# Kernel tuning notes

Measured on AMD Instinct MI355X. Metric: run time of the kernel, lower is better.

## Reference

```python
import jax, jax.numpy as jnp
import numpy as np

N = 50000   # nodes
D = 256     # embed_dim
H = 256     # hidden_dim
E = 250000  # edges per relation type
T = 3       # edge types
NEG_SLOPE = 0.2  # PyG GATConv default


def setup_inputs() -> dict:
    key = jax.random.key(0)
    ks = jax.random.split(key, 12)
    s = lambda k, shape: jax.random.normal(k, shape, jnp.float32) * 0.05
    z = jax.random.normal(ks[0], (N, D), jnp.float32)
    ei = jax.random.randint(ks[1], (T, 2, E), 0, N, dtype=jnp.int32)
    W1 = s(ks[2], (T, D, H)); as1 = s(ks[3], (T, H)); ad1 = s(ks[4], (T, H))
    b1 = jnp.zeros((T, H), jnp.float32)
    W2 = s(ks[5], (T, H, H)); as2 = s(ks[6], (T, H)); ad2 = s(ks[7], (T, H))
    b2 = jnp.zeros((T, H), jnp.float32)
    Wh = s(ks[8], (H, 1)); bh = jnp.zeros((1,), jnp.float32)
    return dict(z=z, ei=ei, W1=W1, as1=as1, ad1=ad1, b1=b1,
                W2=W2, as2=as2, ad2=ad2, b2=b2, Wh=Wh, bh=bh)


def gat_conv(x, ei, W, a_s, a_d, b):
    # PyG GATConv, heads=1, no self loops: h = x W; e_ij = leaky_relu(a_s.h_j + a_d.h_i)
    # alpha = softmax over incoming edges of node i; out_i = sum_j alpha_ij h_j + bias
    src, dst = ei[0], ei[1]
    n = x.shape[0]
    h = x @ W                              # [N, H]
    a_src = h @ a_s                        # [N]
    a_dst = h @ a_d                        # [N]
    e = jax.nn.leaky_relu(a_src[src] + a_dst[dst], NEG_SLOPE)   # [E]
    m = jax.ops.segment_max(e, dst, num_segments=n)             # per-dst max
    ex = jnp.exp(e - m[dst])
    den = jax.ops.segment_sum(ex, dst, num_segments=n)
    alpha = ex / den[dst]                                       # [E]
    out = jax.ops.segment_sum(h[src] * alpha[:, None], dst, num_segments=n)
    return out + b


def layer(x, ei, W, a_s, a_d, b):
    # sum of per-type GATConv outputs, then ReLU (matches module)
    outs = jax.vmap(lambda e_, W_, s_, d_, b_: gat_conv(x, e_, W_, s_, d_, b_))(ei, W, a_s, a_d, b)
    return jax.nn.relu(outs.sum(0))


def reference(z, ei, W1, as1, ad1, b1, W2, as2, ad2, b2, Wh, bh):
    h1 = layer(z, ei, W1, as1, ad1, b1)
    h2 = layer(h1, ei, W2, as2, ad2, b2)
    return jax.nn.sigmoid(h2 @ Wh + bh).squeeze(-1)   # [N]
```

## Files before the change

### kernel.cpp

```cpp
#include <hip/hip_runtime.h>

#define GAT_N 50000
#define GAT_D 256
#define GAT_T 3
#define GAT_E 250000
#define GAT_B (GAT_T*GAT_N)
#define GAT_TOTE (GAT_T*GAT_E)
#define GAT_COLS (GAT_T*GAT_D)
#define GAT_SLOPE 0.2f

typedef unsigned short u16;
typedef unsigned int u32;
typedef __attribute__((ext_vector_type(8))) short s16x8;
typedef __attribute__((ext_vector_type(8))) __bf16 bf16x8;
typedef __attribute__((ext_vector_type(4))) float f32x4;
typedef __attribute__((ext_vector_type(4))) u32 u32x4;

__device__ __forceinline__ u16 f2bf(float f) {
    u32 x = __builtin_bit_cast(u32, f);
    u32 r = (x + 0x7fffu + ((x >> 16) & 1u)) >> 16;
    return (u16)r;
}
__device__ __forceinline__ float lo16(u32 w) {
    return __builtin_bit_cast(float, w << 16);
}
__device__ __forceinline__ float hi16(u32 w) {
    return __builtin_bit_cast(float, w & 0xffff0000u);
}

__global__ void gat_prep(const float* __restrict__ W1, const float* __restrict__ W2,
                         const float* __restrict__ z, const float* __restrict__ b1,
                         const float* __restrict__ b2, u16* __restrict__ WT1b,
                         u16* __restrict__ WT2b, u16* __restrict__ zb,
                         u32* __restrict__ cnt, u32* __restrict__ total,
                         float* __restrict__ bias3)
{
    int idx = blockIdx.x * 256 + threadIdx.x;
    if (idx == 0) *total = 0u;
    if (idx < GAT_T * GAT_D * GAT_D) {
        int t = idx >> 16, r = idx & 65535;
        int d = r >> 8, h = r & 255;
        WT1b[t * 65536 + h * 256 + d] = f2bf(W1[idx]);
        WT2b[t * 65536 + h * 256 + d] = f2bf(W2[idx]);
    }
    if (idx < GAT_B) cnt[idx] = 0u;
    if (idx < 2 * GAT_D) {
        const float* bb = (idx < GAT_D) ? b1 : b2;
        int c = idx & 255;
        bias3[idx] = bb[c] + bb[GAT_D + c] + bb[2 * GAT_D + c];
    }
    if (idx < GAT_N * GAT_D / 4) {
        f32x4 v = ((const f32x4*)z)[idx];
        ushort4 pk;
        pk.x = f2bf(v.x); pk.y = f2bf(v.y); pk.z = f2bf(v.z); pk.w = f2bf(v.w);
        ((ushort4*)zb)[idx] = pk;
    }
}

__global__ void gat_hist(const int* __restrict__ ei, u32* __restrict__ cnt) {
    int idx = blockIdx.x * 256 + threadIdx.x;
    if (idx >= GAT_TOTE) return;
    int t = idx / GAT_E;
    int e = idx - t * GAT_E;
    int dst = ei[t * 2 * GAT_E + GAT_E + e];
    atomicAdd(&cnt[dst * GAT_T + t], 1u);
}

__global__ void gat_alloc(const u32* __restrict__ cnt, u32* __restrict__ pos2,
                          u32* __restrict__ degp, u32* __restrict__ cur,
                          u32* __restrict__ total)
{
    int n = blockIdx.x * 256 + threadIdx.x;
    if (n >= GAT_N) return;
    u32 c0 = cnt[3 * n], c1 = cnt[3 * n + 1], c2 = cnt[3 * n + 2];
    u32 p = atomicAdd(total, c0 + c1 + c2);
    pos2[n] = p;
    degp[n] = c0 | (c1 << 8) | (c2 << 16);
    cur[3 * n]     = p;
    cur[3 * n + 1] = p + c0;
    cur[3 * n + 2] = p + c0 + c1;
}

__global__ void gat_scatter(const int* __restrict__ ei, u32* __restrict__ cur,
                            int* __restrict__ psrc)
{
    int idx = blockIdx.x * 256 + threadIdx.x;
    if (idx >= GAT_TOTE) return;
    int t = idx / GAT_E;
    int e = idx - t * GAT_E;
    int src = ei[t * 2 * GAT_E + e];
    int dst = ei[t * 2 * GAT_E + GAT_E + e];
    u32 slot = atomicAdd(&cur[dst * GAT_T + t], 1u);
    psrc[slot] = t * GAT_N + src;
}

__global__ __launch_bounds__(256) void gat_gemm(
    const u16* __restrict__ A, const u16* __restrict__ WTb,
    u16* __restrict__ H, const float* __restrict__ as_in,
    const float* __restrict__ ad_in, float* __restrict__ part_src,
    float* __restrict__ part_dst)
{
    int lin = blockIdx.x;
    int g   = lin / 48;
    int rem = lin - g * 48;
    int bc  = rem >> 3;
    int br  = (g << 3) + (rem & 7);
    if (br >= 391) return;

    __shared__ u16 Als[128 * 64];
    __shared__ u16 Bls[128 * 64];
    int tid  = threadIdx.x;
    int wave = tid >> 6, lane = tid & 63;
    int quad = lane >> 4, l16 = lane & 15;
    int wm = wave & 1, wn = wave >> 1;
    int lrow = lane >> 3;
    int swz  = ((lane & 7) ^ lrow) * 8;

    size_t arow0 = (size_t)br * 128;
    size_t brow0 = (size_t)bc * 128;

    f32x4 acc[4][4] = {};

    for (int ks = 0; ks < 4; ++ks) {
        int k0 = ks * 64;
        #pragma unroll
        for (int r = 0; r < 4; ++r) {
            int srow = r * 32 + wave * 8 + lrow;
            const u16* gA = A   + (arow0 + srow) * GAT_D + k0 + swz;
            const u16* gB = WTb + (brow0 + srow) * GAT_D + k0 + swz;
            u16* lA = Als + r * 2048 + wave * 512;
            u16* lB = Bls + r * 2048 + wave * 512;
#if defined(__has_builtin) && __has_builtin(__builtin_amdgcn_global_load_lds)
            __builtin_amdgcn_global_load_lds(
                (const __attribute__((address_space(1))) void*)gA,
                (__attribute__((address_space(3))) void*)lA, 16, 0, 0);
            __builtin_amdgcn_global_load_lds(
                (const __attribute__((address_space(1))) void*)gB,
                (__attribute__((address_space(3))) void*)lB, 16, 0, 0);
#else
            *(s16x8*)(lA + lane * 8) = *(const s16x8*)gA;
            *(s16x8*)(lB + lane * 8) = *(const s16x8*)gB;
#endif
        }
        __syncthreads();

        #pragma unroll
        for (int kk = 0; kk < 2; ++kk) {
            int csw8 = ((kk * 4 + quad) ^ (l16 & 7)) * 8;
            bf16x8 af[4], bf[4];
            #pragma unroll
            for (int i = 0; i < 4; ++i) {
                af[i] = __builtin_bit_cast(bf16x8,
                    *(const s16x8*)(Als + (wm * 64 + i * 16 + l16) * 64 + csw8));
                bf[i] = __builtin_bit_cast(bf16x8,
                    *(const s16x8*)(Bls + (wn * 64 + i * 16 + l16) * 64 + csw8));
            }
            #pragma unroll
            for (int i = 0; i < 4; ++i)
                #pragma unroll
                for (int j = 0; j < 4; ++j)
                    acc[i][j] = __builtin_amdgcn_mfma_f32_16x16x32_bf16(
                        af[i], bf[j], acc[i][j], 0, 0, 0);
        }
        __syncthreads();
    }

    int gcol0 = bc * 128 + wn * 64;
    int t   = gcol0 >> 8;
    int ch0 = gcol0 & 255;
    int c64 = (bc << 1) | wn;
    u16* Ht = H + (size_t)t * GAT_N * GAT_D;
    int rowb = br * 128 + wm * 64 + quad * 4;
    #pragma unroll
    for (int i = 0; i < 4; ++i) {
        #pragma unroll
        for (int j = 0; j < 4; ++j) {
            int ch = ch0 + j * 16 + l16;
            #pragma unroll
            for (int r = 0; r < 4; ++r) {
                int row = rowb + i * 16 + r;
                if (row < GAT_N) Ht[(size_t)row * GAT_D + ch] = f2bf(acc[i][j][r]);
            }
        }
    }

    float asv[4], adv[4];
    #pragma unroll
    for (int j = 0; j < 4; ++j) {
        int ch = ch0 + j * 16 + l16;
        asv[j] = as_in[t * GAT_D + ch];
        adv[j] = ad_in[t * GAT_D + ch];
    }
    #pragma unroll
    for (int i = 0; i < 4; ++i) {
        float ps[4] = {}, pd[4] = {};
        #pragma unroll
        for (int j = 0; j < 4; ++j) {
            f32x4 a = acc[i][j];
            #pragma unroll
            for (int r = 0; r < 4; ++r) {
                ps[r] += a[r] * asv[j];
                pd[r] += a[r] * adv[j];
            }
        }
        #pragma unroll
        for (int d = 1; d < 16; d <<= 1) {
            #pragma unroll
            for (int r = 0; r < 4; ++r) {
                ps[r] += __shfl_xor(ps[r], d);
                pd[r] += __shfl_xor(pd[r], d);
            }
        }
        if (l16 == 0) {
            int row = rowb + i * 16;
            #pragma unroll
            for (int r = 0; r < 4; ++r) {
                if (row + r < GAT_N) {
                    part_src[(size_t)c64 * GAT_N + row + r] = ps[r];
                    part_dst[(size_t)c64 * GAT_N + row + r] = pd[r];
                }
            }
        }
    }
}

__global__ void gat_sum(const float* __restrict__ part_src,
                        const float* __restrict__ part_dst,
                        float* __restrict__ a_src, float* __restrict__ a_dst)
{
    int idx = blockIdx.x * 256 + threadIdx.x;
    if (idx >= GAT_B) return;
    int t = idx / GAT_N;
    int n = idx - t * GAT_N;
    const float* ps = part_src + (size_t)4 * t * GAT_N;
    const float* pd = part_dst + (size_t)4 * t * GAT_N;
    a_src[idx] = ps[n] + ps[GAT_N + n] + ps[2 * GAT_N + n] + ps[3 * GAT_N + n];
    a_dst[idx] = pd[n] + pd[GAT_N + n] + pd[2 * GAT_N + n] + pd[3 * GAT_N + n];
}

__global__ __launch_bounds__(256) void gat_gather(
    const u32* __restrict__ pos2, const u32* __restrict__ degp,
    const int* __restrict__ psrc, const float* __restrict__ a_src,
    const float* __restrict__ a_dst, const u16* __restrict__ Hfb,
    const float* __restrict__ bias3, const float* __restrict__ Wh,
    const float* __restrict__ bh, int layer, u16* __restrict__ x2b,
    float* __restrict__ out)
{
    int n = blockIdx.x * 4 + (threadIdx.x >> 6);
    if (n >= GAT_N) return;
    int lane = threadIdx.x & 63;
    int half = lane >> 5, l32 = lane & 31;

    u32 o0 = pos2[n];
    u32 dp = degp[n];
    int d0 = dp & 255, d1 = (dp >> 8) & 255;
    int dtot = d0 + d1 + ((dp >> 16) & 255);
    if (dtot > 64) dtot = 64;

    int  j     = lane;
    bool valid = j < dtot;
    int  tj    = (j >= d0) + (j >= d0 + d1);
    int  rs    = valid ? psrc[o0 + j] : 0;
    float as   = a_src[rs];
    float adn  = a_dst[tj * GAT_N + n];
    float e = as + adn;
    e = (e > 0.f) ? e : GAT_SLOPE * e;
    float ex = valid ? __expf(e) : 0.f;

    float s0 = (tj == 0) ? ex : 0.f;
    float s1 = (tj == 1) ? ex : 0.f;
    float s2 = (tj == 2) ? ex : 0.f;
    #pragma unroll
    for (int d = 1; d < 64; d <<= 1) {
        s0 += __shfl_xor(s0, d);
        s1 += __shfl_xor(s1, d);
        s2 += __shfl_xor(s2, d);
    }
    float den = (tj == 0) ? s0 : ((tj == 1) ? s1 : s2);
    float alv = valid ? ex / den : 0.f;

    float r[8] = {};
    const u16* Hb = Hfb + l32 * 8;
    for (int k0 = 0; k0 < dtot; k0 += 8) {
        float al[4]; u32x4 w[4];
        #pragma unroll
        for (int u = 0; u < 4; ++u) {
            int j2 = k0 + 2 * u + half;
            float a = __shfl(alv, j2);
            int   rv = __shfl(rs, j2);
            bool  v = j2 < dtot;
            al[u] = v ? a : 0.f;
            rv = v ? rv : 0;
            w[u] = *(const u32x4*)(Hb + (size_t)rv * GAT_D);
        }
        #pragma unroll
        for (int u = 0; u < 4; ++u) {
            r[0] += al[u] * lo16(w[u].x); r[1] += al[u] * hi16(w[u].x);
            r[2] += al[u] * lo16(w[u].y); r[3] += al[u] * hi16(w[u].y);
            r[4] += al[u] * lo16(w[u].z); r[5] += al[u] * hi16(w[u].z);
            r[6] += al[u] * lo16(w[u].w); r[7] += al[u] * hi16(w[u].w);
        }
    }
    #pragma unroll
    for (int i = 0; i < 8; ++i) r[i] += __shfl_xor(r[i], 32);

    int c0 = l32 * 8;
    const float* b3 = bias3 + layer * GAT_D;
    float v[8];
    #pragma unroll
    for (int i = 0; i < 8; ++i) v[i] = fmaxf(r[i] + b3[c0 + i], 0.f);

    if (layer == 0) {
        if (half == 0) {
            u16 pk[8];
            #pragma unroll
            for (int i = 0; i < 8; ++i) pk[i] = f2bf(v[i]);
            *(s16x8*)(x2b + (size_t)n * GAT_D + c0) = *(s16x8*)pk;
        }
    } else {
        float wsum = 0.f;
        #pragma unroll
        for (int i = 0; i < 8; ++i) wsum += v[i] * Wh[c0 + i];
        #pragma unroll
        for (int d2 = 1; d2 < 32; d2 <<= 1) wsum += __shfl_xor(wsum, d2);
        if (lane == 0) out[n] = 1.0f / (1.0f + __expf(-(wsum + bh[0])));
    }
}

__global__ void PyGTypeSpecificGAT_80075370266775_kernel() {}

extern "C" void kernel_launch(void* const* d_in, const int* in_sizes, int n_in,
                              void* d_out, int out_size, void* d_ws, size_t ws_size,
                              hipStream_t stream)
{
    (void)in_sizes; (void)n_in; (void)out_size; (void)ws_size;
    const float* z   = (const float*)d_in[0];
    const int*   ei  = (const int*)d_in[1];
    const float* W1  = (const float*)d_in[2];
    const float* as1 = (const float*)d_in[3];
    const float* ad1 = (const float*)d_in[4];
    const float* b1  = (const float*)d_in[5];
    const float* W2  = (const float*)d_in[6];
    const float* as2 = (const float*)d_in[7];
    const float* ad2 = (const float*)d_in[8];
    const float* b2  = (const float*)d_in[9];
    const float* Wh  = (const float*)d_in[10];
    const float* bh  = (const float*)d_in[11];
    float* out = (float*)d_out;

    char* p = (char*)d_ws;
    u16*  Hfb  = (u16*)p;  p += (size_t)GAT_T * GAT_N * GAT_D * 2;
    u16*  x2b  = (u16*)p;  p += (size_t)GAT_N * GAT_D * 2;
    u16*  zb   = (u16*)p;  p += (size_t)GAT_N * GAT_D * 2;
    float* part_src = (float*)p; p += (size_t)12 * GAT_N * 4;
    float* part_dst = (float*)p; p += (size_t)12 * GAT_N * 4;
    float* a_src = (float*)p; p += (size_t)GAT_B * 4;
    float* a_dst = (float*)p; p += (size_t)GAT_B * 4;
    u32*  cnt  = (u32*)p;  p += (size_t)GAT_B * 4;
    u32*  cur  = (u32*)p;  p += (size_t)GAT_B * 4;
    u32*  pos2 = (u32*)p;  p += (size_t)GAT_N * 4;
    u32*  degp = (u32*)p;  p += (size_t)GAT_N * 4;
    u32*  total = (u32*)p; p += 256;
    int*  psrc = (int*)p;  p += (size_t)GAT_TOTE * 4;
    u16*  WT1b = (u16*)p;  p += (size_t)GAT_COLS * GAT_D * 2;
    u16*  WT2b = (u16*)p;  p += (size_t)GAT_COLS * GAT_D * 2;
    float* bias3 = (float*)p; p += 2 * GAT_D * 4;

    const int NODE_BLKS = (GAT_N + 255) / 256;
    const int EDGE_BLKS = (GAT_TOTE + 255) / 256;
    const int BUCK_BLKS = (GAT_B + 255) / 256;
    const int PREP_BLKS = (GAT_N * GAT_D / 4 + 255) / 256;

    gat_prep<<<PREP_BLKS, 256, 0, stream>>>(W1, W2, z, b1, b2, WT1b, WT2b,
                                            zb, cnt, total, bias3);
    gat_hist<<<EDGE_BLKS, 256, 0, stream>>>(ei, cnt);
    gat_alloc<<<NODE_BLKS, 256, 0, stream>>>(cnt, pos2, degp, cur, total);
    gat_scatter<<<EDGE_BLKS, 256, 0, stream>>>(ei, cur, psrc);

    const int GEMM_BLKS = 49 * 48;
    const int GATH_BLKS = GAT_N / 4;

    for (int layer = 0; layer < 2; ++layer) {
        const u16*   A   = (layer == 0) ? zb   : x2b;
        const u16*   WTb = (layer == 0) ? WT1b : WT2b;
        const float* as_ = (layer == 0) ? as1  : as2;
        const float* ad_ = (layer == 0) ? ad1  : ad2;

        gat_gemm<<<GEMM_BLKS, 256, 0, stream>>>(A, WTb, Hfb, as_, ad_,
                                                part_src, part_dst);
        gat_sum<<<BUCK_BLKS, 256, 0, stream>>>(part_src, part_dst,
                                               a_src, a_dst);
        gat_gather<<<GATH_BLKS, 256, 0, stream>>>(pos2, degp, psrc,
                                                  a_src, a_dst, Hfb, bias3,
                                                  Wh, bh, layer, x2b, out);
    }
}
```

Before: 428.7 us.

## Double-buffer GEMM LDS tiles to overlap global loads with MFMA

Splits the A/B shared-memory tiles into two buffers and prefetches the next K-slice into the alternate buffer while MFMAs run on the current one. Explicit vmcnt waits and raw s_barrier calls replace __syncthreads, so the load for step k+1 overlaps compute on step k. LDS use doubles to 64KB per block, which may reduce occupancy. The hand-written vmcnt counts assume exactly 8 outstanding loads per stage and would be wrong on the non-builtin fallback path.

```diff
diff --git a/kernel.cpp b/kernel.cpp
--- a/kernel.cpp
+++ b/kernel.cpp
@@ -107,8 +107,8 @@
     int br  = (g << 3) + (rem & 7);
     if (br >= 391) return;
 
-    __shared__ u16 Als[128 * 64];
-    __shared__ u16 Bls[128 * 64];
+    __shared__ u16 Als[2][128 * 64];
+    __shared__ u16 Bls[2][128 * 64];
     int tid  = threadIdx.x;
     int wave = tid >> 6, lane = tid & 63;
     int quad = lane >> 4, l16 = lane & 15;
@@ -119,17 +119,15 @@
     size_t arow0 = (size_t)br * 128;
     size_t brow0 = (size_t)bc * 128;
 
-    f32x4 acc[4][4] = {};
-
-    for (int ks = 0; ks < 4; ++ks) {
+    auto STAGE = [&](int buf, int ks) {
         int k0 = ks * 64;
         #pragma unroll
         for (int r = 0; r < 4; ++r) {
             int srow = r * 32 + wave * 8 + lrow;
             const u16* gA = A   + (arow0 + srow) * GAT_D + k0 + swz;
             const u16* gB = WTb + (brow0 + srow) * GAT_D + k0 + swz;
-            u16* lA = Als + r * 2048 + wave * 512;
-            u16* lB = Bls + r * 2048 + wave * 512;
+            u16* lA = &Als[buf][r * 2048 + wave * 512];
+            u16* lB = &Bls[buf][r * 2048 + wave * 512];
 #if defined(__has_builtin) && __has_builtin(__builtin_amdgcn_global_load_lds)
             __builtin_amdgcn_global_load_lds(
                 (const __attribute__((address_space(1))) void*)gA,
@@ -138,11 +136,25 @@
                 (const __attribute__((address_space(1))) void*)gB,
                 (__attribute__((address_space(3))) void*)lB, 16, 0, 0);
 #else
-            *(s16x8*)(lA + lane * 8) = *(const s16x8*)gA;
-            *(s16x8*)(lB + lane * 8) = *(const s16x8*)gB;
+            *(s16x8*)(&Als[buf][r * 2048 + wave * 512] + lane * 8) = *(const s16x8*)gA;
+            *(s16x8*)(&Bls[buf][r * 2048 + wave * 512] + lane * 8) = *(const s16x8*)gB;
 #endif
         }
-        __syncthreads();
+    };
+
+    f32x4 acc[4][4] = {};
+
+    STAGE(0, 0);
+    #pragma unroll
+    for (int ks = 0; ks < 4; ++ks) {
+        int cur = ks & 1;
+        if (ks < 3) {
+            STAGE(cur ^ 1, ks + 1);
+            asm volatile("s_waitcnt vmcnt(8)" ::: "memory");
+        } else {
+            asm volatile("s_waitcnt vmcnt(0)" ::: "memory");
+        }
+        __builtin_amdgcn_s_barrier();
 
         #pragma unroll
         for (int kk = 0; kk < 2; ++kk) {
@@ -151,9 +163,9 @@
             #pragma unroll
             for (int i = 0; i < 4; ++i) {
                 af[i] = __builtin_bit_cast(bf16x8,
-                    *(const s16x8*)(Als + (wm * 64 + i * 16 + l16) * 64 + csw8));
+                    *(const s16x8*)(&Als[cur][(wm * 64 + i * 16 + l16) * 64 + csw8]));
                 bf[i] = __builtin_bit_cast(bf16x8,
-                    *(const s16x8*)(Bls + (wn * 64 + i * 16 + l16) * 64 + csw8));
+                    *(const s16x8*)(&Bls[cur][(wn * 64 + i * 16 + l16) * 64 + csw8]));
             }
             #pragma unroll
             for (int i = 0; i < 4; ++i)
@@ -162,7 +174,8 @@
                     acc[i][j] = __builtin_amdgcn_mfma_f32_16x16x32_bf16(
                         af[i], bf[j], acc[i][j], 0, 0, 0);
         }
-        __syncthreads();
+        if (ks < 3)
+            __builtin_amdgcn_s_barrier();
     }
 
     int gcol0 = bc * 128 + wn * 64;
```

Result: no change. 420.8 us (-1.8%).
